# Kernel tuning notes

Hardware: AMD Instinct MI355X
Metric: run time of the kernel (lower is better)

The kernel has to match this reference:

```python
import jax, jax.numpy as jnp
import numpy as np

B, S, H = 2, 2048, 2048
NH, NKV, DH = 16, 4, 128
E, TOPK, MI = 8, 2, 1408
EPS = 1e-6


def _rms_norm(x, w):
    var = jnp.mean(x.astype(jnp.float32) ** 2, axis=-1, keepdims=True)
    return (x * jax.lax.rsqrt(var + EPS)).astype(x.dtype) * w


def _rotate_half(x):
    x1, x2 = jnp.split(x, 2, axis=-1)
    return jnp.concatenate([-x2, x1], axis=-1)


def setup_inputs() -> dict:
    key = jax.random.key(0)
    ks = jax.random.split(key, 12)
    hidden_states = jax.random.normal(ks[0], (B, S, H), dtype=jnp.float32)
    # real RoPE angles: [S, DH] broadcast to [B, S, DH]
    inv_freq = 1.0 / (10000.0 ** (np.arange(0, DH, 2, dtype=np.float32) / DH))
    pos = np.arange(S, dtype=np.float32)
    freqs = np.einsum('s,d->sd', pos, inv_freq)          # [S, DH/2]
    emb = np.concatenate([freqs, freqs], axis=-1)        # [S, DH]
    cos = jnp.broadcast_to(jnp.cos(emb)[None], (B, S, DH)).astype(jnp.float32)
    sin = jnp.broadcast_to(jnp.sin(emb)[None], (B, S, DH)).astype(jnp.float32)
    sc = 0.02
    wq = jax.random.normal(ks[1], (H, NH * DH), dtype=jnp.float32) * sc
    wk = jax.random.normal(ks[2], (H, NKV * DH), dtype=jnp.float32) * sc
    wv = jax.random.normal(ks[3], (H, NKV * DH), dtype=jnp.float32) * sc
    wo = jax.random.normal(ks[4], (NH * DH, H), dtype=jnp.float32) * sc
    ln1_w = jnp.ones((H,), dtype=jnp.float32)
    ln2_w = jnp.ones((H,), dtype=jnp.float32)
    router_w = jax.random.normal(ks[5], (H, E), dtype=jnp.float32) * sc
    gate_w = jax.random.normal(ks[6], (E, H, MI), dtype=jnp.float32) * sc
    up_w = jax.random.normal(ks[7], (E, H, MI), dtype=jnp.float32) * sc
    down_w = jax.random.normal(ks[8], (E, MI, H), dtype=jnp.float32) * sc
    return dict(hidden_states=hidden_states, cos=cos, sin=sin, wq=wq, wk=wk,
                wv=wv, wo=wo, ln1_w=ln1_w, ln2_w=ln2_w, router_w=router_w,
                gate_w=gate_w, up_w=up_w, down_w=down_w)


def _forward(hidden_states, cos, sin, wq, wk, wv, wo, ln1_w, ln2_w,
             router_w, gate_w, up_w, down_w):
    residual = hidden_states
    x = _rms_norm(hidden_states, ln1_w)
    # ---- attention with RoPE + GQA ----
    q = (x @ wq).reshape(B, S, NH, DH).transpose(0, 2, 1, 3)    # [B,NH,S,DH]
    k = (x @ wk).reshape(B, S, NKV, DH).transpose(0, 2, 1, 3)   # [B,NKV,S,DH]
    v = (x @ wv).reshape(B, S, NKV, DH).transpose(0, 2, 1, 3)
    c = cos[:, None]  # [B,1,S,DH]
    s = sin[:, None]
    q = q * c + _rotate_half(q) * s
    k = k * c + _rotate_half(k) * s
    groups = NH // NKV
    k = jnp.repeat(k, groups, axis=1)   # [B,NH,S,DH]
    v = jnp.repeat(v, groups, axis=1)
    scale = 1.0 / jnp.sqrt(jnp.asarray(DH, dtype=q.dtype))
    scores = jnp.einsum('bhqd,bhkd->bhqk', q, k) * scale
    attn = jax.nn.softmax(scores, axis=-1)
    out = jnp.einsum('bhqk,bhkd->bhqd', attn, v)
    out = out.transpose(0, 2, 1, 3).reshape(B, S, NH * DH) @ wo
    hidden = residual + out
    # ---- MoE ----
    residual = hidden
    x = _rms_norm(hidden, ln2_w).reshape(-1, H)                  # [T,H]
    logits = x @ router_w                                        # [T,E]
    probs = jax.nn.softmax(logits.astype(jnp.float32), axis=-1)
    topv, topi = jax.lax.top_k(probs, TOPK)                      # [T,K]
    topv = topv / jnp.sum(topv, axis=-1, keepdims=True)          # norm_topk_prob
    T = x.shape[0]
    combine = jnp.zeros((T, E), dtype=jnp.float32)
    combine = combine.at[jnp.arange(T)[:, None], topi].add(topv)
    combine = combine.astype(x.dtype)                            # [T,E]
    g = jax.nn.silu(jnp.einsum('th,ehi->eti', x, gate_w))
    u = jnp.einsum('th,ehi->eti', x, up_w)
    expert_out = jnp.einsum('eti,eih->eth', g * u, down_w)       # [E,T,H]
    moe_out = jnp.einsum('eth,te->th', expert_out, combine)
    return residual + moe_out.reshape(B, S, H)


def reference(hidden_states, cos, sin, wq, wk, wv, wo, ln1_w, ln2_w,
              router_w, gate_w, up_w, down_w):
    return _forward(hidden_states, cos, sin, wq, wk, wv, wo, ln1_w, ln2_w,
                    router_w, gate_w, up_w, down_w)
```

## Files before the change

### kernel.cpp

```cpp
#include <hip/hip_runtime.h>

typedef unsigned short u16;
typedef u16 u16x8 __attribute__((ext_vector_type(8)));
typedef short s16x8 __attribute__((ext_vector_type(8)));
typedef float f32x4 __attribute__((ext_vector_type(4)));

#define TT 4096
#define HH 2048

__device__ __forceinline__ float bf2f(u16 u){ union{unsigned int i; float f;} v; v.i = ((unsigned int)u)<<16; return v.f; }
__device__ __forceinline__ u16 f2bf(float f){ union{float f; unsigned int i;} v; v.f = f; unsigned int r = v.i + 0x7fffu + ((v.i>>16)&1u); return (u16)(r>>16); }

__global__ __launch_bounds__(256) void tconv(const float* __restrict__ in, u16* __restrict__ out,
    int R, int C, int ldo, long inB, long outB){
  __shared__ float t[32][33];
  const float* inp = in + (long)blockIdx.z * inB;
  u16* outp = out + (long)blockIdx.z * outB;
  int c0 = blockIdx.x*32, r0 = blockIdx.y*32;
  int tx = threadIdx.x, ty = threadIdx.y;
  #pragma unroll
  for (int j=0;j<4;j++){
    int r = r0 + ty + j*8;
    t[ty+j*8][tx] = inp[(long)r*C + (c0+tx)];
  }
  __syncthreads();
  #pragma unroll
  for (int j=0;j<4;j++){
    int c = c0 + ty + j*8;
    outp[(long)c*ldo + (r0+tx)] = f2bf(t[tx][ty+j*8]);
  }
}

__global__ __launch_bounds__(256) void vtrans(const u16* __restrict__ qkv, u16* __restrict__ vt){
  __shared__ u16 t[32][34];
  int bg = blockIdx.z; int b = bg>>2, g = bg&3;
  int s0 = blockIdx.x*32, d0 = blockIdx.y*32;
  int tx = threadIdx.x, ty = threadIdx.y;
  #pragma unroll
  for (int j=0;j<4;j++){
    t[ty+j*8][tx] = qkv[(long)(b*2048 + s0+ty+j*8)*3072 + 2560 + g*128 + d0+tx];
  }
  __syncthreads();
  #pragma unroll
  for (int j=0;j<4;j++){
    vt[((long)bg*128 + d0+ty+j*8)*2048 + s0+tx] = t[tx][ty+j*8];
  }
}

__global__ __launch_bounds__(256) void rmsnorm_k(const float* __restrict__ in, const float* __restrict__ w,
                                                 u16* __restrict__ out){
  long t = blockIdx.x;
  const float* row = in + t*HH;
  int tid = threadIdx.x;
  float x[8]; float ss = 0.f;
  #pragma unroll
  for (int i=0;i<8;i++){ x[i] = row[tid + i*256]; ss += x[i]*x[i]; }
  #pragma unroll
  for (int o=1;o<64;o<<=1) ss += __shfl_xor(ss, o, 64);
  __shared__ float sw[4];
  if ((tid&63)==0) sw[tid>>6] = ss;
  __syncthreads();
  ss = sw[0]+sw[1]+sw[2]+sw[3];
  float sc = rsqrtf(ss*(1.f/HH) + 1e-6f);
  #pragma unroll
  for (int i=0;i<8;i++){ int idx = tid+i*256; out[t*HH+idx] = f2bf(x[i]*sc*w[idx]); }
}

template<int EPI, bool GATHER, bool GROUPED>
__global__ __launch_bounds__(256) void gemm_bt(
    const u16* __restrict__ A, const u16* __restrict__ B,
    int K, int M_fixed,
    const int* __restrict__ counts, const int* __restrict__ offsets,
    const int* __restrict__ lists, const float* __restrict__ wlists,
    long strideB,
    u16* __restrict__ Cbf, int ldc,
    float* __restrict__ Cf1, float* __restrict__ Cf2,
    const float* __restrict__ Resid)
{
  int e = GROUPED ? blockIdx.z : 0;
  int cnt = GROUPED ? counts[e] : M_fixed;
  int m0 = blockIdx.y * 128;
  if (m0 >= cnt) return;
  int n0 = blockIdx.x * 128;
  int base = GROUPED ? offsets[e] : 0;
  const u16* B2 = B + (long)e * strideB;

  __shared__ u16 lA[128*40];
  __shared__ u16 lB[128*40];

  int tid = threadIdx.x;
  int wave = tid>>6, lane = tid&63;
  int wm = (wave>>1)*64, wn = (wave&1)*64;
  int quad = lane>>4, l16 = lane&15;

  int kA = (tid&3)*8;
  int r0a = m0 + (tid>>2), r1a = r0a + 64;
  if (r0a >= cnt) r0a = cnt-1;
  if (r1a >= cnt) r1a = cnt-1;
  long ga0, ga1;
  if constexpr (GATHER){ ga0 = (long)lists[e*4096 + r0a]*K; ga1 = (long)lists[e*4096 + r1a]*K; }
  else if constexpr (GROUPED){ ga0 = (long)(base + r0a)*K; ga1 = (long)(base + r1a)*K; }
  else { ga0 = (long)r0a*K; ga1 = (long)r1a*K; }
  ga0 += kA; ga1 += kA;
  long gb0 = (long)(n0 + (tid>>2))*K + kA;
  long gb1 = gb0 + 64L*K;
  int lr = (tid>>2)*40 + kA;

  f32x4 zero = {0.f,0.f,0.f,0.f};
  f32x4 acc[4][4];
  #pragma unroll
  for (int i=0;i<4;i++)
    #pragma unroll
    for (int j=0;j<4;j++) acc[i][j] = zero;

  for (int kt=0; kt<K; kt+=32){
    *(u16x8*)(&lA[lr])        = *(const u16x8*)(A + ga0 + kt);
    *(u16x8*)(&lA[lr + 64*40])= *(const u16x8*)(A + ga1 + kt);
    *(u16x8*)(&lB[lr])        = *(const u16x8*)(B2 + gb0 + kt);
    *(u16x8*)(&lB[lr + 64*40])= *(const u16x8*)(B2 + gb1 + kt);
    __syncthreads();
    s16x8 af[4], bfr[4];
    #pragma unroll
    for (int i=0;i<4;i++){
      af[i]  = *(const s16x8*)(&lA[(wm + i*16 + l16)*40 + quad*8]);
      bfr[i] = *(const s16x8*)(&lB[(wn + i*16 + l16)*40 + quad*8]);
    }
    #pragma unroll
    for (int i=0;i<4;i++)
      #pragma unroll
      for (int j=0;j<4;j++)
        acc[i][j] = __builtin_amdgcn_mfma_f32_16x16x32_bf16(af[i], bfr[j], acc[i][j], 0,0,0);
    __syncthreads();
  }

  #pragma unroll
  for (int i=0;i<4;i++){
    #pragma unroll
    for (int j=0;j<4;j++){
      #pragma unroll
      for (int rr=0; rr<4; rr++){
        int row = m0 + wm + i*16 + quad*4 + rr;
        int col = n0 + wn + j*16 + l16;
        float v = acc[i][j][rr];
        if constexpr (EPI==0){
          if (row < cnt) Cbf[(long)(base+row)*ldc + col] = f2bf(v);
        } else if constexpr (EPI==1){
          long idx = (long)row*ldc + col;
          float o = v + Resid[idx];
          Cf1[idx] = o; Cf2[idx] = o;
        } else {
          if (row < cnt){
            int tk = lists[e*4096 + row];
            float wgt = wlists[e*4096 + row];
            atomicAdd(&Cf1[(long)tk*ldc + col], wgt*v);
          }
        }
      }
    }
  }
}

__global__ __launch_bounds__(256) void rope_k(u16* __restrict__ qkv, const float* __restrict__ cosb,
                                              const float* __restrict__ sinb){
  long t = blockIdx.x;
  for (int p = threadIdx.x; p < 1280; p += 256){
    int head = p>>6, d = p&63;
    long base = t*3072 + (head<16 ? head*128 : 2048 + (head-16)*128);
    float c1 = cosb[t*128+d],    s1 = sinb[t*128+d];
    float c2 = cosb[t*128+d+64], s2 = sinb[t*128+d+64];
    float x1 = bf2f(qkv[base+d]), x2 = bf2f(qkv[base+d+64]);
    qkv[base+d]    = f2bf(x1*c1 - x2*s1);
    qkv[base+d+64] = f2bf(x2*c2 + x1*s2);
  }
}

__global__ __launch_bounds__(256,2) void attn_k(const u16* __restrict__ qkv, const u16* __restrict__ vt,
                                                u16* __restrict__ out){
  __shared__ u16 lK [64*136];
  __shared__ u16 lVt[128*72];
  __shared__ u16 lP [4*32*72];
  int qt = blockIdx.x, h = blockIdx.y, b = blockIdx.z;
  int g = h>>2;
  int tid = threadIdx.x, wave = tid>>6, lane = tid&63;
  int quad = lane>>4, l16 = lane&15;
  long qbase = (long)b*2048 + qt*128;
  const float c = 0.08838834764831845f * 1.4426950408889634f;

  s16x8 qf[2][4];
  #pragma unroll
  for (int i=0;i<2;i++){
    long tok = qbase + wave*32 + i*16 + l16;
    #pragma unroll
    for (int kk=0;kk<4;kk++)
      qf[i][kk] = *(const s16x8*)(qkv + tok*3072 + h*128 + kk*32 + quad*8);
  }

  f32x4 O[2][8];
  #pragma unroll
  for (int i=0;i<2;i++)
    #pragma unroll
    for (int f=0;f<8;f++) O[i][f] = (f32x4){0.f,0.f,0.f,0.f};
  float mS[2][4], lS[2][4];
  #pragma unroll
  for (int i=0;i<2;i++)
    #pragma unroll
    for (int rr=0;rr<4;rr++){ mS[i][rr] = -1e30f; lS[i][rr] = 0.f; }

  const u16* kbase  = qkv + (long)b*2048*3072 + 2048 + g*128;
  const u16* vtbase = vt + ((long)(b*4+g))*128*2048;
  int koct = tid&15, krow = tid>>4;
  int voct = tid&7,  vrow = tid>>3;
  u16* lPw = lP + wave*32*72;

  for (int kt=0; kt<2048; kt+=64){
    __syncthreads();
    #pragma unroll
    for (int j2=0;j2<4;j2++){
      int r = krow + j2*16;
      *(u16x8*)(lK + r*136 + koct*8) = *(const u16x8*)(kbase + (long)(kt+r)*3072 + koct*8);
    }
    #pragma unroll
    for (int j2=0;j2<4;j2++){
      int d = vrow + j2*32;
      *(u16x8*)(lVt + d*72 + voct*8) = *(const u16x8*)(vtbase + (long)d*2048 + kt + voct*8);
    }
    __syncthreads();

    f32x4 S[2][4];
    #pragma unroll
    for (int i=0;i<2;i++)
      #pragma unroll
      for (int j=0;j<4;j++) S[i][j] = (f32x4){0.f,0.f,0.f,0.f};
    #pragma unroll
    for (int kk=0;kk<4;kk++){
      s16x8 bk[4];
      #pragma unroll
      for (int j=0;j<4;j++)
        bk[j] = *(const s16x8*)(lK + (j*16+l16)*136 + kk*32 + quad*8);
      #pragma unroll
      for (int i=0;i<2;i++)
        #pragma unroll
        for (int j=0;j<4;j++)
          S[i][j] = __builtin_amdgcn_mfma_f32_16x16x32_bf16(qf[i][kk], bk[j], S[i][j], 0,0,0);
    }

    #pragma unroll
    for (int i=0;i<2;i++){
      float al[4];
      #pragma unroll
      for (int rr=0;rr<4;rr++){
        float v = fmaxf(fmaxf(S[i][0][rr],S[i][1][rr]), fmaxf(S[i][2][rr],S[i][3][rr]));
        v = fmaxf(v, __shfl_xor(v,1,64));
        v = fmaxf(v, __shfl_xor(v,2,64));
        v = fmaxf(v, __shfl_xor(v,4,64));
        v = fmaxf(v, __shfl_xor(v,8,64));
        float mn = fmaxf(v, mS[i][rr]);
        al[rr] = exp2f((mS[i][rr]-mn)*c);
        mS[i][rr] = mn;
        float rs = 0.f;
        #pragma unroll
        for (int j=0;j<4;j++){
          float p = exp2f((S[i][j][rr]-mn)*c);
          S[i][j][rr] = p; rs += p;
        }
        rs += __shfl_xor(rs,1,64);
        rs += __shfl_xor(rs,2,64);
        rs += __shfl_xor(rs,4,64);
        rs += __shfl_xor(rs,8,64);
        lS[i][rr] = lS[i][rr]*al[rr] + rs;
      }
      #pragma unroll
      for (int j=0;j<4;j++)
        #pragma unroll
        for (int rr=0;rr<4;rr++)
          lPw[(i*16 + quad*4 + rr)*72 + j*16 + l16] = f2bf(S[i][j][rr]);
      #pragma unroll
      for (int f=0;f<8;f++)
        #pragma unroll
        for (int rr=0;rr<4;rr++) O[i][f][rr] *= al[rr];
    }

    #pragma unroll
    for (int kk=0;kk<2;kk++){
      s16x8 ap[2];
      #pragma unroll
      for (int i=0;i<2;i++)
        ap[i] = *(const s16x8*)(lPw + (i*16+l16)*72 + kk*32 + quad*8);
      #pragma unroll
      for (int f=0;f<8;f++){
        s16x8 bv = *(const s16x8*)(lVt + (f*16+l16)*72 + kk*32 + quad*8);
        O[0][f] = __builtin_amdgcn_mfma_f32_16x16x32_bf16(ap[0], bv, O[0][f], 0,0,0);
        O[1][f] = __builtin_amdgcn_mfma_f32_16x16x32_bf16(ap[1], bv, O[1][f], 0,0,0);
      }
    }
  }

  #pragma unroll
  for (int i=0;i<2;i++){
    float inv[4];
    #pragma unroll
    for (int rr=0;rr<4;rr++) inv[rr] = 1.f/lS[i][rr];
    #pragma unroll
    for (int f=0;f<8;f++)
      #pragma unroll
      for (int rr=0;rr<4;rr++){
        long tok = qbase + wave*32 + i*16 + quad*4 + rr;
        out[tok*2048 + h*128 + f*16 + l16] = f2bf(O[i][f][rr]*inv[rr]);
      }
  }
}

__global__ __launch_bounds__(256) void router_k(const float* __restrict__ h2, const float* __restrict__ w2,
    const float* __restrict__ rw, int* counts, int* lists, float* wlists){
  long t = blockIdx.x;
  const float* row = h2 + t*HH;
  int tid = threadIdx.x;
  float x[8]; float ss = 0.f;
  #pragma unroll
  for (int i=0;i<8;i++){ int idx = tid + i*256; x[i]=row[idx]; ss += x[i]*x[i]; }
  #pragma unroll
  for (int o=1;o<64;o<<=1) ss += __shfl_xor(ss,o,64);
  __shared__ float ssw[4];
  int wave = tid>>6, lane = tid&63;
  if (lane==0) ssw[wave]=ss;
  __syncthreads();
  ss = ssw[0]+ssw[1]+ssw[2]+ssw[3];
  float sc = rsqrtf(ss*(1.f/HH) + 1e-6f);
  float part[8] = {0,0,0,0,0,0,0,0};
  #pragma unroll
  for (int i=0;i<8;i++){
    int idx = tid + i*256;
    float xn = x[i]*sc*w2[idx];
    const float* r8 = rw + (long)idx*8;
    #pragma unroll
    for (int e2=0;e2<8;e2++) part[e2] += xn*r8[e2];
  }
  #pragma unroll
  for (int e2=0;e2<8;e2++)
    #pragma unroll
    for (int o=1;o<64;o<<=1) part[e2] += __shfl_xor(part[e2],o,64);
  __shared__ float pw[4][8];
  if (lane==0){
    #pragma unroll
    for (int e2=0;e2<8;e2++) pw[wave][e2]=part[e2];
  }
  __syncthreads();
  if (tid==0){
    float lg[8];
    #pragma unroll
    for (int e2=0;e2<8;e2++) lg[e2]=pw[0][e2]+pw[1][e2]+pw[2][e2]+pw[3][e2];
    float mx = lg[0];
    #pragma unroll
    for (int e2=1;e2<8;e2++) mx = fmaxf(mx, lg[e2]);
    float pz[8];
    #pragma unroll
    for (int e2=0;e2<8;e2++) pz[e2] = __expf(lg[e2]-mx);
    int i1 = 0;
    #pragma unroll
    for (int e2=1;e2<8;e2++) if (pz[e2] > pz[i1]) i1 = e2;
    int i2 = (i1==0) ? 1 : 0;
    #pragma unroll
    for (int e2=0;e2<8;e2++) if (e2!=i1 && pz[e2] > pz[i2]) i2 = e2;
    float v1 = pz[i1], v2 = pz[i2];
    float inv = 1.f/(v1+v2);
    int p1 = atomicAdd(&counts[i1],1);
    lists[i1*4096+p1] = (int)t; wlists[i1*4096+p1] = v1*inv;
    int p2 = atomicAdd(&counts[i2],1);
    lists[i2*4096+p2] = (int)t; wlists[i2*4096+p2] = v2*inv;
  }
}

__global__ void zero8(int* p){ if (threadIdx.x < 8) p[threadIdx.x] = 0; }
__global__ void prefix8(const int* __restrict__ counts, int* __restrict__ offs){
  if (threadIdx.x==0){ int o=0; for (int e=0;e<8;e++){ offs[e]=o; o+=counts[e]; } }
}

__global__ __launch_bounds__(256) void silu_k(const u16* __restrict__ graw, u16* __restrict__ gu){
  long row = blockIdx.x;
  const u16* gr = graw + row*2816;
  u16* o = gu + row*1408;
  for (int i = threadIdx.x; i < 1408; i += 256){
    float g = bf2f(gr[i]);
    float u = bf2f(gr[1408+i]);
    float s = g / (1.f + __expf(-g));
    o[i] = f2bf(s*u);
  }
}

static constexpr long OFF_WQKV  = 0;
static constexpr long OFF_WO    = 12582912;
static constexpr long OFF_GUW   = 20971520;
static constexpr long OFF_DW    = 113246208;
static constexpr long ARENA     = 159383552;
static constexpr long OFF_XBF   = ARENA;
static constexpr long OFF_QKV   = ARENA + 16777216;
static constexpr long OFF_ATT   = ARENA + 41943040;
static constexpr long OFF_GURAW = ARENA;
static constexpr long OFF_H2    = 218103808;
static constexpr long OFF_GU    = 218103808;
static constexpr long OFF_X2    = 251658240;
static constexpr long OFF_CNT   = 268435456;
static constexpr long OFF_OFFS  = 268435488;
static constexpr long OFF_LIST  = 268435520;
static constexpr long OFF_WL    = 268566592;

extern "C" void kernel_launch(void* const* d_in, const int* in_sizes, int n_in,
                              void* d_out, int out_size, void* d_ws, size_t ws_size,
                              hipStream_t stream) {
  const float* hs   = (const float*)d_in[0];
  const float* cosb = (const float*)d_in[1];
  const float* sinb = (const float*)d_in[2];
  const float* wq   = (const float*)d_in[3];
  const float* wk   = (const float*)d_in[4];
  const float* wv   = (const float*)d_in[5];
  const float* wo   = (const float*)d_in[6];
  const float* ln1  = (const float*)d_in[7];
  const float* ln2  = (const float*)d_in[8];
  const float* rw   = (const float*)d_in[9];
  const float* gw   = (const float*)d_in[10];
  const float* uw   = (const float*)d_in[11];
  const float* dw   = (const float*)d_in[12];
  float* out = (float*)d_out;
  char* ws = (char*)d_ws;

  u16* wqkv_bt = (u16*)(ws + OFF_WQKV);
  u16* wo_bt   = (u16*)(ws + OFF_WO);
  u16* guw_bt  = (u16*)(ws + OFF_GUW);
  u16* dw_bt   = (u16*)(ws + OFF_DW);
  u16* x_bf    = (u16*)(ws + OFF_XBF);
  u16* qkv_bf  = (u16*)(ws + OFF_QKV);
  u16* att_bf  = (u16*)(ws + OFF_ATT);
  u16* guraw   = (u16*)(ws + OFF_GURAW);
  float* h2    = (float*)(ws + OFF_H2);
  u16* gu      = (u16*)(ws + OFF_GU);
  u16* x2_bf   = (u16*)(ws + OFF_X2);
  u16* vt      = (u16*)(ws + OFF_XBF);
  int* counts  = (int*)(ws + OFF_CNT);
  int* offs    = (int*)(ws + OFF_OFFS);
  int* lists   = (int*)(ws + OFF_LIST);
  float* wlists= (float*)(ws + OFF_WL);

  dim3 tb(32,8);
  tconv<<<dim3(64,64,1),tb,0,stream>>>(wq, wqkv_bt,                2048,2048,2048, 0,0);
  tconv<<<dim3(16,64,1),tb,0,stream>>>(wk, wqkv_bt + 2048L*2048,   2048, 512,2048, 0,0);
  tconv<<<dim3(16,64,1),tb,0,stream>>>(wv, wqkv_bt + 2560L*2048,   2048, 512,2048, 0,0);
  tconv<<<dim3(64,64,1),tb,0,stream>>>(wo, wo_bt,                  2048,2048,2048, 0,0);
  tconv<<<dim3(44,64,8),tb,0,stream>>>(gw, guw_bt,                 2048,1408,2048, 2048L*1408, 2816L*2048);
  tconv<<<dim3(44,64,8),tb,0,stream>>>(uw, guw_bt + 1408L*2048,    2048,1408,2048, 2048L*1408, 2816L*2048);
  tconv<<<dim3(64,44,8),tb,0,stream>>>(dw, dw_bt,                  1408,2048,1408, 1408L*2048, 2048L*1408);

  rmsnorm_k<<<TT,256,0,stream>>>(hs, ln1, x_bf);

  gemm_bt<0,false,false><<<dim3(24,32,1),256,0,stream>>>(x_bf, wqkv_bt, 2048, 4096,
      nullptr,nullptr,nullptr,nullptr, 0, qkv_bf, 3072, nullptr,nullptr,nullptr);

  rope_k<<<TT,256,0,stream>>>(qkv_bf, cosb, sinb);

  vtrans<<<dim3(64,4,8),tb,0,stream>>>(qkv_bf, vt);

  attn_k<<<dim3(16,16,2),256,0,stream>>>(qkv_bf, vt, att_bf);

  gemm_bt<1,false,false><<<dim3(16,32,1),256,0,stream>>>(att_bf, wo_bt, 2048, 4096,
      nullptr,nullptr,nullptr,nullptr, 0, nullptr, 2048, h2, out, hs);

  rmsnorm_k<<<TT,256,0,stream>>>(h2, ln2, x2_bf);
  zero8<<<1,64,0,stream>>>(counts);
  router_k<<<TT,256,0,stream>>>(h2, ln2, rw, counts, lists, wlists);
  prefix8<<<1,64,0,stream>>>(counts, offs);

  gemm_bt<0,true,true><<<dim3(22,32,8),256,0,stream>>>(x2_bf, guw_bt, 2048, 0,
      counts, offs, lists, wlists, 2816L*2048, guraw, 2816, nullptr,nullptr,nullptr);

  silu_k<<<8192,256,0,stream>>>(guraw, gu);

  gemm_bt<2,false,true><<<dim3(16,32,8),256,0,stream>>>(gu, dw_bt, 1408, 0,
      counts, offs, lists, wlists, 2048L*1408, nullptr, 2048, out, nullptr, nullptr);

  (void)in_sizes; (void)n_in; (void)out_size; (void)ws_size;
}
```

Measured before the change: 1.155 ms.

## Load GEMM tiles directly into LDS with XOR-swizzled layout

Replaces the register-staged global-to-shared tile copies in the bf16 MFMA GEMM with direct global_load_lds 16-byte transfers, one per lane into a wave-contiguous LDS region. Since direct LDS loads fix the destination layout, the padded 40-element row stride is dropped for a dense 32-element stride, and an XOR swizzle on the k-chunk offset avoids bank conflicts on the fragment reads. This removes VGPR staging and the separate LDS write instructions, but the loop still has no double buffering, and correctness depends on the swizzle on the write side matching the one on the read side.

Result: faster. 1.132 ms (-2.0%).

```diff
diff --git a/kernel.cpp b/kernel.cpp
--- a/kernel.cpp
+++ b/kernel.cpp
@@ -10,6 +10,11 @@
 
 __device__ __forceinline__ float bf2f(u16 u){ union{unsigned int i; float f;} v; v.i = ((unsigned int)u)<<16; return v.f; }
 __device__ __forceinline__ u16 f2bf(float f){ union{float f; unsigned int i;} v; v.f = f; unsigned int r = v.i + 0x7fffu + ((v.i>>16)&1u); return (u16)(r>>16); }
+
+__device__ __forceinline__ void gl_lds16(const u16* g, u16* l){
+  __builtin_amdgcn_global_load_lds((const __attribute__((address_space(1))) unsigned int*)g,
+                                   (__attribute__((address_space(3))) unsigned int*)l, 16, 0, 0);
+}
 
 __global__ __launch_bounds__(256) void tconv(const float* __restrict__ in, u16* __restrict__ out,
     int R, int C, int ldo, long inB, long outB){
@@ -85,26 +90,33 @@
   int base = GROUPED ? offsets[e] : 0;
   const u16* B2 = B + (long)e * strideB;
 
-  __shared__ u16 lA[128*40];
-  __shared__ u16 lB[128*40];
+  __shared__ u16 lA[128*32];
+  __shared__ u16 lB[128*32];
 
   int tid = threadIdx.x;
   int wave = tid>>6, lane = tid&63;
   int wm = (wave>>1)*64, wn = (wave&1)*64;
   int quad = lane>>4, l16 = lane&15;
 
-  int kA = (tid&3)*8;
-  int r0a = m0 + (tid>>2), r1a = r0a + 64;
+  int rloc = lane>>2;
+  int koff = ((lane&3) ^ ((lane>>3)&3))*8;
+  int r0a = m0 + wave*16 + rloc;
+  int r1a = r0a + 64;
   if (r0a >= cnt) r0a = cnt-1;
   if (r1a >= cnt) r1a = cnt-1;
   long ga0, ga1;
   if constexpr (GATHER){ ga0 = (long)lists[e*4096 + r0a]*K; ga1 = (long)lists[e*4096 + r1a]*K; }
   else if constexpr (GROUPED){ ga0 = (long)(base + r0a)*K; ga1 = (long)(base + r1a)*K; }
   else { ga0 = (long)r0a*K; ga1 = (long)r1a*K; }
-  ga0 += kA; ga1 += kA;
-  long gb0 = (long)(n0 + (tid>>2))*K + kA;
+  ga0 += koff; ga1 += koff;
+  long gb0 = (long)(n0 + wave*16 + rloc)*K + koff;
   long gb1 = gb0 + 64L*K;
-  int lr = (tid>>2)*40 + kA;
+  u16* lA0 = lA + wave*16*32; u16* lA1 = lA0 + 64*32;
+  u16* lB0 = lB + wave*16*32; u16* lB1 = lB0 + 64*32;
+
+  int sw8 = (quad ^ ((l16>>1)&3))*8;
+  int aoff = (wm + l16)*32 + sw8;
+  int boff = (wn + l16)*32 + sw8;
 
   f32x4 zero = {0.f,0.f,0.f,0.f};
   f32x4 acc[4][4];
@@ -114,16 +126,16 @@
     for (int j=0;j<4;j++) acc[i][j] = zero;
 
   for (int kt=0; kt<K; kt+=32){
-    *(u16x8*)(&lA[lr])        = *(const u16x8*)(A + ga0 + kt);
-    *(u16x8*)(&lA[lr + 64*40])= *(const u16x8*)(A + ga1 + kt);
-    *(u16x8*)(&lB[lr])        = *(const u16x8*)(B2 + gb0 + kt);
-    *(u16x8*)(&lB[lr + 64*40])= *(const u16x8*)(B2 + gb1 + kt);
+    gl_lds16(A  + ga0 + kt, lA0);
+    gl_lds16(A  + ga1 + kt, lA1);
+    gl_lds16(B2 + gb0 + kt, lB0);
+    gl_lds16(B2 + gb1 + kt, lB1);
     __syncthreads();
     s16x8 af[4], bfr[4];
     #pragma unroll
     for (int i=0;i<4;i++){
-      af[i]  = *(const s16x8*)(&lA[(wm + i*16 + l16)*40 + quad*8]);
-      bfr[i] = *(const s16x8*)(&lB[(wn + i*16 + l16)*40 + quad*8]);
+      af[i]  = *(const s16x8*)(&lA[aoff + i*512]);
+      bfr[i] = *(const s16x8*)(&lB[boff + i*512]);
     }
     #pragma unroll
     for (int i=0;i<4;i++)
```
